# Performance work log

Hardware: AMD Instinct MI355X
Metric: run time of the kernel (lower is better)

Reference implementation:

```python
import jax, jax.numpy as jnp
import numpy as np

B, N, M, K, C = 2, 4096, 4096, 32, 64
RADIUS = 0.08


def _ball_query(d2, radius, k):
    # d2: (B, N, M) squared distances. Returns (B, N, k) int32 indices of the
    # first k in-radius neighbors (in index order); empty slots are filled with
    # the first found neighbor (or 0 if none), matching standard ball_query.
    m = d2.shape[-1]
    mask = d2 < radius * radius
    ar = jnp.arange(m, dtype=jnp.int32)
    key = jnp.where(mask, ar, ar + m)          # in-radius indices sort first
    neg_vals, _ = jax.lax.top_k(-key, k)       # k smallest keys
    vals = -neg_vals
    valid = vals < m
    raw = vals % m
    fill = raw[..., :1]                        # first neighbor (0 if none)
    return jnp.where(valid, raw, fill)


def setup_inputs() -> dict:
    key = jax.random.key(0)
    ks = jax.random.split(key, 9)
    points = jax.random.uniform(ks[0], (B, 3, N), dtype=jnp.float32)
    knnpoints = jax.random.uniform(ks[1], (B, 3, M), dtype=jnp.float32)
    feat = jax.random.normal(ks[2], (B, C, M), dtype=jnp.float32)
    w1 = jax.random.normal(ks[3], (128, C + 4), dtype=jnp.float32) * 0.05
    b1 = jnp.zeros((128,), jnp.float32)
    w2 = jax.random.normal(ks[4], (64, 128), dtype=jnp.float32) * 0.05
    b2 = jnp.zeros((64,), jnp.float32)
    w3 = jax.random.normal(ks[5], (64, 64), dtype=jnp.float32) * 0.05
    b3 = jnp.zeros((64,), jnp.float32)
    return {"points": points, "knnpoints": knnpoints, "feat": feat,
            "w1": w1, "b1": b1, "w2": w2, "b2": b2, "w3": w3, "b3": b3}


def reference(points, knnpoints, feat, w1, b1, w2, b2, w3, b3):
    # pairwise squared distances (B, N, M), computed once and reused by
    # ball_query and ChamferLoss
    pe = jnp.sum(points ** 2, axis=1)                       # (B, N)
    ke = jnp.sum(knnpoints ** 2, axis=1)                    # (B, M)
    cross = jnp.einsum('bdn,bdm->bnm', points, knnpoints)
    d2 = jnp.maximum(pe[:, :, None] + ke[:, None, :] - 2.0 * cross, 0.0)

    idx = _ball_query(jax.lax.stop_gradient(d2), RADIUS, K)  # (B, N, K)

    # gather neighbor coords / features: knnpoints[j, :, idx[j]]
    nb = jax.vmap(lambda p, i: p[:, i])(knnpoints, idx)      # (B, 3, N, K)
    nf = jax.vmap(lambda f, i: f[:, i])(feat, idx)           # (B, C, N, K)

    # relation features (neighbor_feature): diff + squared distance
    diff = nb - points[:, :, :, None]                        # (B, 3, N, K)
    dist = jnp.sum(diff ** 2, axis=1, keepdims=True)         # (B, 1, N, K)
    x = jnp.concatenate([nf, diff, dist], axis=1)            # (B, C+4, N, K)

    # SharedMLP: 1x1 conv stacks + ReLU
    h = jax.nn.relu(jnp.einsum('oc,bcnk->bonk', w1, x) + b1[None, :, None, None])
    h = jax.nn.relu(jnp.einsum('oc,bcnk->bonk', w2, h) + b2[None, :, None, None])
    h = jax.nn.relu(jnp.einsum('oc,bcnk->bonk', w3, h) + b3[None, :, None, None])
    agg = jnp.sum(h, axis=3)                                 # (B, 64, N)

    # ChamferLoss between points and knnpoints
    cd = jnp.sqrt(1e-6 + d2)
    loss = jnp.min(cd, axis=1).mean() + jnp.min(cd, axis=2).mean()
    return agg, loss
```

## Files before the change

kernel.cpp:

```cpp
#include <hip/hip_runtime.h>
#include <cstdint>

#define BB 2
#define NN 4096
#define MM 4096
#define KK 32
#define CC 64
#define R2C 0.0064f

typedef _Float16 v8h __attribute__((ext_vector_type(8)));
typedef _Float16 v4h __attribute__((ext_vector_type(4)));
typedef float    v4f __attribute__((ext_vector_type(4)));

#define TC  64
#define XS  104
#define H1S 136
#define H2S 72

#define NBLK_COLMIN 512
#define NBLK_MLP    4096
#define NBLK_TOTAL  4608

__launch_bounds__(256)
__global__ void prep_kernel(const float* __restrict__ knn,
                            const float* __restrict__ feat,
                            const float* __restrict__ w1,
                            const float* __restrict__ w2,
                            const float* __restrict__ w3,
                            _Float16* __restrict__ featH,
                            _Float16* __restrict__ w1h,
                            _Float16* __restrict__ w2h,
                            _Float16* __restrict__ w3h,
                            float4* __restrict__ knnP) {
    __shared__ __align__(16) float tl[64][65];
    int t = threadIdx.x, blk = blockIdx.x;

    if (blk < 128) {
        int b = blk >> 6;
        int m0 = (blk & 63) * 64;
        int mi = t & 63, cq = t >> 6;
        const float* src = feat + (size_t)b * CC * MM;
#pragma unroll
        for (int r = 0; r < 16; ++r) {
            int c = cq * 16 + r;
            tl[mi][c] = src[(size_t)c * MM + m0 + mi];
        }
        __syncthreads();
        int ci = t & 63, mq = t >> 6;
        _Float16* dst = featH + ((size_t)b * MM + m0) * CC;
#pragma unroll
        for (int r = 0; r < 16; ++r) {
            int mm2 = mq * 16 + r;
            dst[(size_t)mm2 * CC + ci] = (_Float16)tl[mm2][ci];
        }
    } else if (blk < 176) {
        int tt = (blk - 128) * 256 + t;
        if (tt < 128 * 96) {
            int r = tt / 96, k = tt - r * 96;
            w1h[tt] = (_Float16)((k < 68) ? w1[r * 68 + k] : 0.0f);
        }
        if (tt < 64 * 128) w2h[tt] = (_Float16)w2[tt];
        if (tt < 64 * 64)  w3h[tt] = (_Float16)w3[tt];
    } else {
        int i0 = (blk - 176) * 256 + t;
#pragma unroll
        for (int j = 0; j < 4; ++j) {
            int i = i0 + 2048 * j;
            int b = i >> 12, m = i & (MM - 1);
            const float* kp = knn + (size_t)b * 3 * MM;
            float x = kp[m], y = kp[MM + m], z = kp[2 * MM + m];
            float e = __fadd_rn(__fadd_rn(__fmul_rn(x, x), __fmul_rn(y, y)),
                                __fmul_rn(z, z));
            knnP[i] = make_float4(x, y, z, e);
        }
    }
}

__launch_bounds__(256, 4)
__global__ void fused_kernel(const float* __restrict__ points,
                             const float4* __restrict__ knnP,
                             const _Float16* __restrict__ featH,
                             const _Float16* __restrict__ w1h, const float* __restrict__ b1,
                             const _Float16* __restrict__ w2h, const float* __restrict__ b2,
                             const _Float16* __restrict__ w3h, const float* __restrict__ b3,
                             float* __restrict__ lossbuf,
                             float* __restrict__ out) {
    __shared__ __align__(16) _Float16 SM[TC * XS + TC * H1S];
    _Float16* X  = SM;
    _Float16* H2 = SM;
    _Float16* H1 = SM + TC * XS;
    __shared__ int   lists[2][4][KK];
    __shared__ int   cnts[2][4];
    __shared__ int   sidx2[2][KK];
    __shared__ float wmin[2][4];

    int t = threadIdx.x;
    int w = t >> 6, lane = t & 63;
    int blk = blockIdx.x;

    if (blk < NBLK_COLMIN) {
        float4* tile = (float4*)SM;
        int m0 = blk * 16;
        int b = blk >> 8;
        const float* pp = points + (size_t)b * 3 * NN;
        const float4* kq = knnP + (size_t)b * MM;
        float4 Kp[4];
#pragma unroll
        for (int p = 0; p < 4; ++p)
            Kp[p] = kq[(m0 & (MM - 1)) + 4 * w + p];
        float mn[4] = {1e30f, 1e30f, 1e30f, 1e30f};

        for (int ch = 0; ch < 4; ++ch) {
            const float* px = pp + ch * 1024;
#pragma unroll
            for (int j = 0; j < 4; ++j) {
                int i = t + 256 * j;
                float x = px[i], y = px[NN + i], z = px[2 * NN + i];
                float e = __fadd_rn(__fadd_rn(__fmul_rn(x, x), __fmul_rn(y, y)),
                                    __fmul_rn(z, z));
                tile[i] = make_float4(x, y, z, e);
            }
            __syncthreads();
#pragma unroll 2
            for (int i = 0; i < 16; ++i) {
                float4 p4 = tile[i * 64 + lane];
#pragma unroll
                for (int p = 0; p < 4; ++p) {
                    float cross = __builtin_fmaf(p4.z, Kp[p].z,
                                  __builtin_fmaf(p4.y, Kp[p].y,
                                                 __fmul_rn(p4.x, Kp[p].x)));
                    float d2 = __fsub_rn(__fadd_rn(p4.w, Kp[p].w),
                                         __fmul_rn(2.0f, cross));
                    mn[p] = fminf(mn[p], d2);
                }
            }
            __syncthreads();
        }

        float lsum = 0.0f;
#pragma unroll
        for (int p = 0; p < 4; ++p) {
            float mv = mn[p];
            for (int off = 32; off > 0; off >>= 1)
                mv = fminf(mv, __shfl_xor(mv, off));
            lsum += sqrtf(1e-6f + fmaxf(mv, 0.0f));
        }
        if (lane == 0) wmin[0][w] = lsum;
        __syncthreads();
        if (t == 0)
            lossbuf[blk] = (wmin[0][0] + wmin[0][1] + wmin[0][2] + wmin[0][3])
                           * (1.0f / (BB * MM));
    } else {
        int point0 = (blk - NBLK_COLMIN) * 2;
        int b = point0 >> 12;
        int n0 = point0 & (NN - 1);
        const float* pp = points + (size_t)b * 3 * NN;
        const float4* kq = knnP + (size_t)b * MM;

        float4 P[2];
#pragma unroll
        for (int p = 0; p < 2; ++p) {
            int n = n0 + p;
            float x = pp[n], y = pp[NN + n], z = pp[2 * NN + n];
            float e = __fadd_rn(__fadd_rn(__fmul_rn(x, x), __fmul_rn(y, y)),
                                __fmul_rn(z, z));
            P[p] = make_float4(x, y, z, e);
        }
        int cnt[2] = {0, 0};
        float mn[2] = {1e30f, 1e30f};
        int mbase = w * 1024 + lane;
#pragma unroll 4
        for (int it = 0; it < 16; ++it) {
            int m = mbase + it * 64;
            float4 k4 = kq[m];
#pragma unroll
            for (int p = 0; p < 2; ++p) {
                float cross = __builtin_fmaf(P[p].z, k4.z,
                              __builtin_fmaf(P[p].y, k4.y,
                                             __fmul_rn(P[p].x, k4.x)));
                float d2 = __fsub_rn(__fadd_rn(P[p].w, k4.w),
                                     __fmul_rn(2.0f, cross));
                mn[p] = fminf(mn[p], d2);
                bool hit = d2 < R2C;
                unsigned long long mask = __ballot(hit);
                if (hit) {
                    int pos = cnt[p] + __builtin_amdgcn_mbcnt_hi(
                                 (unsigned)(mask >> 32),
                                 __builtin_amdgcn_mbcnt_lo((unsigned)mask, 0));
                    if (pos < KK) lists[p][w][pos] = m;
                }
                cnt[p] += __popcll(mask);
            }
        }
#pragma unroll
        for (int p = 0; p < 2; ++p) {
            if (lane == 0) cnts[p][w] = cnt[p];
            float mv = mn[p];
            for (int off = 32; off > 0; off >>= 1)
                mv = fminf(mv, __shfl_xor(mv, off));
            if (lane == 0) wmin[p][w] = mv;
        }
        __syncthreads();

        if (w == 0) {
            int p = lane >> 5, k = lane & 31;
            int c0 = cnts[p][0], c1 = cnts[p][1], c2 = cnts[p][2], c3 = cnts[p][3];
            int o1 = c0, o2 = o1 + c1, o3 = o2 + c2, total = o3 + c3;
            int fillv = 0;
            if (c0 > 0)      fillv = lists[p][0][0];
            else if (c1 > 0) fillv = lists[p][1][0];
            else if (c2 > 0) fillv = lists[p][2][0];
            else if (c3 > 0) fillv = lists[p][3][0];
            int src, base;
            if (k < o1)      { src = 0; base = 0;  }
            else if (k < o2) { src = 1; base = o1; }
            else if (k < o3) { src = 2; base = o2; }
            else             { src = 3; base = o3; }
            int v = (k < total) ? lists[p][src][k - base] : fillv;
            sidx2[p][k] = v;
            if (lane == 0) {
                float r0 = fminf(fminf(wmin[0][0], wmin[0][1]),
                                 fminf(wmin[0][2], wmin[0][3]));
                float r1 = fminf(fminf(wmin[1][0], wmin[1][1]),
                                 fminf(wmin[1][2], wmin[1][3]));
                lossbuf[blk] = (sqrtf(1e-6f + fmaxf(r0, 0.0f)) +
                                sqrtf(1e-6f + fmaxf(r1, 0.0f)))
                               * (1.0f / (BB * NN));
            }
        }
        __syncthreads();

        {
            int col = t >> 2, h = t & 3;
            int pl = col >> 5, kk = col & 31;
            int n = n0 + pl;
            int id = sidx2[pl][kk];
            const v8h* src = (const v8h*)(featH + ((size_t)(b * MM + id)) * CC) + h * 2;
            v8h f0 = src[0], f1 = src[1];
            v8h* dst = (v8h*)(X + col * XS) + h * 2;
            dst[0] = f0; dst[1] = f1;
            v8h mv = {(_Float16)0.f, (_Float16)0.f, (_Float16)0.f, (_Float16)0.f,
                      (_Float16)0.f, (_Float16)0.f, (_Float16)0.f, (_Float16)0.f};
            if (h == 0) {
                float4 Pm = pl ? P[1] : P[0];
                float4 k4 = kq[id];
                float dx = k4.x - Pm.x, dy = k4.y - Pm.y, dz = k4.z - Pm.z;
                float dd = __fadd_rn(__fadd_rn(__fmul_rn(dx, dx), __fmul_rn(dy, dy)),
                                     __fmul_rn(dz, dz));
                mv[0] = (_Float16)dx; mv[1] = (_Float16)dy;
                mv[2] = (_Float16)dz; mv[3] = (_Float16)dd;
            }
            *((v8h*)(X + col * XS + 64) + h) = mv;
        }

        int quad = lane >> 4, lc = lane & 15;

        v8h a1[2][3], a2[4], a3[2];
#pragma unroll
        for (int rt = 0; rt < 2; ++rt)
#pragma unroll
            for (int ks = 0; ks < 3; ++ks)
                a1[rt][ks] = *(const v8h*)(w1h + (32 * w + 16 * rt + lc) * 96 + 32 * ks + 8 * quad);
#pragma unroll
        for (int ks = 0; ks < 4; ++ks)
            a2[ks] = *(const v8h*)(w2h + (16 * w + lc) * 128 + 32 * ks + 8 * quad);
#pragma unroll
        for (int ks = 0; ks < 2; ++ks)
            a3[ks] = *(const v8h*)(w3h + (16 * w + lc) * 64 + 32 * ks + 8 * quad);

        v4f bias1a = *(const v4f*)(b1 + 32 * w + 4 * quad);
        v4f bias1b = *(const v4f*)(b1 + 32 * w + 16 + 4 * quad);
        v4f bias2  = *(const v4f*)(b2 + 16 * w + 4 * quad);
        v4f bias3  = *(const v4f*)(b3 + 16 * w + 4 * quad);

        __syncthreads();

#pragma unroll 1
        for (int ct = 0; ct < 4; ++ct) {
            int colb = 16 * ct + lc;
            v4f acc0 = bias1a, acc1 = bias1b;
#pragma unroll
            for (int ks = 0; ks < 3; ++ks) {
                v8h bx = *(const v8h*)(X + colb * XS + 32 * ks + 8 * quad);
                acc0 = __builtin_amdgcn_mfma_f32_16x16x32_f16(a1[0][ks], bx, acc0, 0, 0, 0);
                acc1 = __builtin_amdgcn_mfma_f32_16x16x32_f16(a1[1][ks], bx, acc1, 0, 0, 0);
            }
            v4h h0, h1v;
#pragma unroll
            for (int r = 0; r < 4; ++r) {
                h0[r]  = (_Float16)fmaxf(acc0[r], 0.0f);
                h1v[r] = (_Float16)fmaxf(acc1[r], 0.0f);
            }
            *(v4h*)(H1 + colb * H1S + 32 * w + 4 * quad)      = h0;
            *(v4h*)(H1 + colb * H1S + 32 * w + 16 + 4 * quad) = h1v;
        }
        __syncthreads();

#pragma unroll 1
        for (int ct = 0; ct < 4; ++ct) {
            int colb = 16 * ct + lc;
            v4f acc = bias2;
#pragma unroll
            for (int ks = 0; ks < 4; ++ks) {
                v8h bx = *(const v8h*)(H1 + colb * H1S + 32 * ks + 8 * quad);
                acc = __builtin_amdgcn_mfma_f32_16x16x32_f16(a2[ks], bx, acc, 0, 0, 0);
            }
            v4h h;
#pragma unroll
            for (int r = 0; r < 4; ++r) h[r] = (_Float16)fmaxf(acc[r], 0.0f);
            *(v4h*)(H2 + colb * H2S + 16 * w + 4 * quad) = h;
        }
        __syncthreads();

#pragma unroll 1
        for (int p = 0; p < 2; ++p) {
            int cA = (2 * p) * 16 + lc, cB = (2 * p + 1) * 16 + lc;
            v4f accA = bias3, accB = bias3;
#pragma unroll
            for (int ks = 0; ks < 2; ++ks) {
                v8h bA = *(const v8h*)(H2 + cA * H2S + 32 * ks + 8 * quad);
                v8h bB = *(const v8h*)(H2 + cB * H2S + 32 * ks + 8 * quad);
                accA = __builtin_amdgcn_mfma_f32_16x16x32_f16(a3[ks], bA, accA, 0, 0, 0);
                accB = __builtin_amdgcn_mfma_f32_16x16x32_f16(a3[ks], bB, accB, 0, 0, 0);
            }
            v4f s;
#pragma unroll
            for (int r = 0; r < 4; ++r)
                s[r] = fmaxf(accA[r], 0.0f) + fmaxf(accB[r], 0.0f);
#pragma unroll
            for (int off = 1; off < 16; off <<= 1) {
#pragma unroll
                for (int r = 0; r < 4; ++r) s[r] += __shfl_xor(s[r], off);
            }
            if (lc == 0) {
                int n = n0 + p;
                int rowb = 16 * w + 4 * quad;
#pragma unroll
                for (int r = 0; r < 4; ++r)
                    out[((size_t)(b * 64 + rowb + r)) * NN + n] = s[r];
            }
        }
    }
}

__launch_bounds__(256)
__global__ void loss_kernel(const float* __restrict__ lossbuf,
                            float* __restrict__ out) {
    __shared__ float ws4[4];
    int t = threadIdx.x;
    float s = 0.0f;
#pragma unroll
    for (int q = 0; q < 18; ++q)
        s += lossbuf[t + 256 * q];
    for (int off = 32; off > 0; off >>= 1) s += __shfl_xor(s, off);
    if ((t & 63) == 0) ws4[t >> 6] = s;
    __syncthreads();
    if (t == 0)
        out[(size_t)BB * 64 * NN] = ws4[0] + ws4[1] + ws4[2] + ws4[3];
}

extern "C" void kernel_launch(void* const* d_in, const int* in_sizes, int n_in,
                              void* d_out, int out_size, void* d_ws, size_t ws_size,
                              hipStream_t stream) {
    const float* points = (const float*)d_in[0];
    const float* knn    = (const float*)d_in[1];
    const float* feat   = (const float*)d_in[2];
    const float* w1 = (const float*)d_in[3];
    const float* b1 = (const float*)d_in[4];
    const float* w2 = (const float*)d_in[5];
    const float* b2 = (const float*)d_in[6];
    const float* w3 = (const float*)d_in[7];
    const float* b3 = (const float*)d_in[8];
    float* out = (float*)d_out;

    char* ws = (char*)d_ws;
    _Float16*  featH   = (_Float16*)ws;
    _Float16*  w1h     = (_Float16*)(ws + 1048576);
    _Float16*  w2h     = (_Float16*)(ws + 1073152);
    _Float16*  w3h     = (_Float16*)(ws + 1089536);
    float4*    knnP    = (float4*)(ws + 1097728);
    float*     lossbuf = (float*)(ws + 1228800);

    prep_kernel<<<184, 256, 0, stream>>>(knn, feat, w1, w2, w3,
                                         featH, w1h, w2h, w3h, knnP);
    fused_kernel<<<NBLK_TOTAL, 256, 0, stream>>>(points, knnP, featH,
                                                 w1h, b1, w2h, b2, w3h, b3,
                                                 lossbuf, out);
    loss_kernel<<<1, 256, 0, stream>>>(lossbuf, out);
}
```

Measured before the change: 131.7 us.

## Load gathered features directly into MFMA operands, dropping the X staging tile

The fused kernel stops staging gathered neighbor features into a shared X tile. Each layer-1 MFMA now reads its B operand straight from global featH rows, and the relative-position metadata is precomputed by wave 0 into a small shared array. This removes the X buffer and one barrier, so shared memory shrinks and launch bounds rise to 5 blocks per CU. It also hoists the weight loads ahead of the ball query, merges the two ballots under a single branch, and vectorizes the featH transpose stores in prep. In exchange, each wave issues uncoalesced global loads inside the MFMA loop, and register pressure rises because the hoisted weights stay live through the search.

Result: no change. 132.6 us (+0.7%).

```diff
diff --git a/kernel.cpp b/kernel.cpp
--- a/kernel.cpp
+++ b/kernel.cpp
@@ -13,7 +13,6 @@
 typedef float    v4f __attribute__((ext_vector_type(4)));
 
 #define TC  64
-#define XS  104
 #define H1S 136
 #define H2S 72
 
@@ -46,12 +45,15 @@
             tl[mi][c] = src[(size_t)c * MM + m0 + mi];
         }
         __syncthreads();
-        int ci = t & 63, mq = t >> 6;
         _Float16* dst = featH + ((size_t)b * MM + m0) * CC;
 #pragma unroll
-        for (int r = 0; r < 16; ++r) {
-            int mm2 = mq * 16 + r;
-            dst[(size_t)mm2 * CC + ci] = (_Float16)tl[mm2][ci];
+        for (int rr = 0; rr < 2; ++rr) {
+            int mm2 = (t >> 3) + 32 * rr;
+            int cj = (t & 7) * 8;
+            v8h v;
+#pragma unroll
+            for (int j = 0; j < 8; ++j) v[j] = (_Float16)tl[mm2][cj + j];
+            *(v8h*)(dst + (size_t)mm2 * CC + cj) = v;
         }
     } else if (blk < 176) {
         int tt = (blk - 128) * 256 + t;
@@ -76,7 +78,7 @@
     }
 }
 
-__launch_bounds__(256, 4)
+__launch_bounds__(256, 5)
 __global__ void fused_kernel(const float* __restrict__ points,
                              const float4* __restrict__ knnP,
                              const _Float16* __restrict__ featH,
@@ -85,14 +87,14 @@
                              const _Float16* __restrict__ w3h, const float* __restrict__ b3,
                              float* __restrict__ lossbuf,
                              float* __restrict__ out) {
-    __shared__ __align__(16) _Float16 SM[TC * XS + TC * H1S];
-    _Float16* X  = SM;
-    _Float16* H2 = SM;
-    _Float16* H1 = SM + TC * XS;
+    __shared__ __align__(16) _Float16 SM[TC * H1S + TC * H2S];
+    _Float16* H1 = SM;
+    _Float16* H2 = SM + TC * H1S;
     __shared__ int   lists[2][4][KK];
     __shared__ int   cnts[2][4];
     __shared__ int   sidx2[2][KK];
     __shared__ float wmin[2][4];
+    __shared__ v4h   meta4[64];
 
     int t = threadIdx.x;
     int w = t >> 6, lane = t & 63;
@@ -157,6 +159,26 @@
         const float* pp = points + (size_t)b * 3 * NN;
         const float4* kq = knnP + (size_t)b * MM;
 
+        int quad = lane >> 4, lc = lane & 15;
+
+        v8h a1[2][3], a2[4], a3[2];
+#pragma unroll
+        for (int rt = 0; rt < 2; ++rt)
+#pragma unroll
+            for (int ks = 0; ks < 3; ++ks)
+                a1[rt][ks] = *(const v8h*)(w1h + (32 * w + 16 * rt + lc) * 96 + 32 * ks + 8 * quad);
+#pragma unroll
+        for (int ks = 0; ks < 4; ++ks)
+            a2[ks] = *(const v8h*)(w2h + (16 * w + lc) * 128 + 32 * ks + 8 * quad);
+#pragma unroll
+        for (int ks = 0; ks < 2; ++ks)
+            a3[ks] = *(const v8h*)(w3h + (16 * w + lc) * 64 + 32 * ks + 8 * quad);
+
+        v4f bias1a = *(const v4f*)(b1 + 32 * w + 4 * quad);
+        v4f bias1b = *(const v4f*)(b1 + 32 * w + 16 + 4 * quad);
+        v4f bias2  = *(const v4f*)(b2 + 16 * w + 4 * quad);
+        v4f bias3  = *(const v4f*)(b3 + 16 * w + 4 * quad);
+
         float4 P[2];
 #pragma unroll
         for (int p = 0; p < 2; ++p) {
@@ -173,23 +195,39 @@
         for (int it = 0; it < 16; ++it) {
             int m = mbase + it * 64;
             float4 k4 = kq[m];
-#pragma unroll
-            for (int p = 0; p < 2; ++p) {
-                float cross = __builtin_fmaf(P[p].z, k4.z,
-                              __builtin_fmaf(P[p].y, k4.y,
-                                             __fmul_rn(P[p].x, k4.x)));
-                float d2 = __fsub_rn(__fadd_rn(P[p].w, k4.w),
-                                     __fmul_rn(2.0f, cross));
-                mn[p] = fminf(mn[p], d2);
-                bool hit = d2 < R2C;
-                unsigned long long mask = __ballot(hit);
-                if (hit) {
-                    int pos = cnt[p] + __builtin_amdgcn_mbcnt_hi(
-                                 (unsigned)(mask >> 32),
-                                 __builtin_amdgcn_mbcnt_lo((unsigned)mask, 0));
-                    if (pos < KK) lists[p][w][pos] = m;
+            float d2a, d2b;
+            {
+                float cross = __builtin_fmaf(P[0].z, k4.z,
+                              __builtin_fmaf(P[0].y, k4.y,
+                                             __fmul_rn(P[0].x, k4.x)));
+                d2a = __fsub_rn(__fadd_rn(P[0].w, k4.w), __fmul_rn(2.0f, cross));
+            }
+            {
+                float cross = __builtin_fmaf(P[1].z, k4.z,
+                              __builtin_fmaf(P[1].y, k4.y,
+                                             __fmul_rn(P[1].x, k4.x)));
+                d2b = __fsub_rn(__fadd_rn(P[1].w, k4.w), __fmul_rn(2.0f, cross));
+            }
+            mn[0] = fminf(mn[0], d2a);
+            mn[1] = fminf(mn[1], d2b);
+            bool hit0 = d2a < R2C, hit1 = d2b < R2C;
+            unsigned long long mk0 = __ballot(hit0);
+            unsigned long long mk1 = __ballot(hit1);
+            if (mk0 | mk1) {
+                if (hit0) {
+                    int pos = cnt[0] + __builtin_amdgcn_mbcnt_hi(
+                                 (unsigned)(mk0 >> 32),
+                                 __builtin_amdgcn_mbcnt_lo((unsigned)mk0, 0));
+                    if (pos < KK) lists[0][w][pos] = m;
                 }
-                cnt[p] += __popcll(mask);
+                cnt[0] += __popcll(mk0);
+                if (hit1) {
+                    int pos = cnt[1] + __builtin_amdgcn_mbcnt_hi(
+                                 (unsigned)(mk1 >> 32),
+                                 __builtin_amdgcn_mbcnt_lo((unsigned)mk1, 0));
+                    if (pos < KK) lists[1][w][pos] = m;
+                }
+                cnt[1] += __popcll(mk1);
             }
         }
 #pragma unroll
@@ -218,6 +256,15 @@
             else             { src = 3; base = o3; }
             int v = (k < total) ? lists[p][src][k - base] : fillv;
             sidx2[p][k] = v;
+            float4 k4 = kq[v];
+            float4 Pm = p ? P[1] : P[0];
+            float dx = k4.x - Pm.x, dy = k4.y - Pm.y, dz = k4.z - Pm.z;
+            float dd = __fadd_rn(__fadd_rn(__fmul_rn(dx, dx), __fmul_rn(dy, dy)),
+                                 __fmul_rn(dz, dz));
+            v4h mv;
+            mv[0] = (_Float16)dx; mv[1] = (_Float16)dy;
+            mv[2] = (_Float16)dz; mv[3] = (_Float16)dd;
+            meta4[lane] = mv;
             if (lane == 0) {
                 float r0 = fminf(fminf(wmin[0][0], wmin[0][1]),
                                  fminf(wmin[0][2], wmin[0][3]));
@@ -230,61 +277,27 @@
         }
         __syncthreads();
 
-        {
-            int col = t >> 2, h = t & 3;
-            int pl = col >> 5, kk = col & 31;
-            int n = n0 + pl;
-            int id = sidx2[pl][kk];
-            const v8h* src = (const v8h*)(featH + ((size_t)(b * MM + id)) * CC) + h * 2;
-            v8h f0 = src[0], f1 = src[1];
-            v8h* dst = (v8h*)(X + col * XS) + h * 2;
-            dst[0] = f0; dst[1] = f1;
-            v8h mv = {(_Float16)0.f, (_Float16)0.f, (_Float16)0.f, (_Float16)0.f,
-                      (_Float16)0.f, (_Float16)0.f, (_Float16)0.f, (_Float16)0.f};
-            if (h == 0) {
-                float4 Pm = pl ? P[1] : P[0];
-                float4 k4 = kq[id];
-                float dx = k4.x - Pm.x, dy = k4.y - Pm.y, dz = k4.z - Pm.z;
-                float dd = __fadd_rn(__fadd_rn(__fmul_rn(dx, dx), __fmul_rn(dy, dy)),
-                                     __fmul_rn(dz, dz));
-                mv[0] = (_Float16)dx; mv[1] = (_Float16)dy;
-                mv[2] = (_Float16)dz; mv[3] = (_Float16)dd;
-            }
-            *((v8h*)(X + col * XS + 64) + h) = mv;
-        }
-
-        int quad = lane >> 4, lc = lane & 15;
-
-        v8h a1[2][3], a2[4], a3[2];
-#pragma unroll
-        for (int rt = 0; rt < 2; ++rt)
-#pragma unroll
-            for (int ks = 0; ks < 3; ++ks)
-                a1[rt][ks] = *(const v8h*)(w1h + (32 * w + 16 * rt + lc) * 96 + 32 * ks + 8 * quad);
-#pragma unroll
-        for (int ks = 0; ks < 4; ++ks)
-            a2[ks] = *(const v8h*)(w2h + (16 * w + lc) * 128 + 32 * ks + 8 * quad);
-#pragma unroll
-        for (int ks = 0; ks < 2; ++ks)
-            a3[ks] = *(const v8h*)(w3h + (16 * w + lc) * 64 + 32 * ks + 8 * quad);
-
-        v4f bias1a = *(const v4f*)(b1 + 32 * w + 4 * quad);
-        v4f bias1b = *(const v4f*)(b1 + 32 * w + 16 + 4 * quad);
-        v4f bias2  = *(const v4f*)(b2 + 16 * w + 4 * quad);
-        v4f bias3  = *(const v4f*)(b3 + 16 * w + 4 * quad);
-
-        __syncthreads();
-
 #pragma unroll 1
         for (int ct = 0; ct < 4; ++ct) {
             int colb = 16 * ct + lc;
+            int id = ((const int*)sidx2)[colb];
+            const _Float16* frow = featH + ((size_t)(b * MM + id)) * CC;
+            v8h bx0 = *(const v8h*)(frow + 8 * quad);
+            v8h bx1 = *(const v8h*)(frow + 32 + 8 * quad);
+            v4h mrow = meta4[colb];
+            v8h bx2 = {(_Float16)0.f, (_Float16)0.f, (_Float16)0.f, (_Float16)0.f,
+                       (_Float16)0.f, (_Float16)0.f, (_Float16)0.f, (_Float16)0.f};
+            if (quad == 0) {
+                bx2[0] = mrow[0]; bx2[1] = mrow[1];
+                bx2[2] = mrow[2]; bx2[3] = mrow[3];
+            }
             v4f acc0 = bias1a, acc1 = bias1b;
-#pragma unroll
-            for (int ks = 0; ks < 3; ++ks) {
-                v8h bx = *(const v8h*)(X + colb * XS + 32 * ks + 8 * quad);
-                acc0 = __builtin_amdgcn_mfma_f32_16x16x32_f16(a1[0][ks], bx, acc0, 0, 0, 0);
-                acc1 = __builtin_amdgcn_mfma_f32_16x16x32_f16(a1[1][ks], bx, acc1, 0, 0, 0);
-            }
+            acc0 = __builtin_amdgcn_mfma_f32_16x16x32_f16(a1[0][0], bx0, acc0, 0, 0, 0);
+            acc1 = __builtin_amdgcn_mfma_f32_16x16x32_f16(a1[1][0], bx0, acc1, 0, 0, 0);
+            acc0 = __builtin_amdgcn_mfma_f32_16x16x32_f16(a1[0][1], bx1, acc0, 0, 0, 0);
+            acc1 = __builtin_amdgcn_mfma_f32_16x16x32_f16(a1[1][1], bx1, acc1, 0, 0, 0);
+            acc0 = __builtin_amdgcn_mfma_f32_16x16x32_f16(a1[0][2], bx2, acc0, 0, 0, 0);
+            acc1 = __builtin_amdgcn_mfma_f32_16x16x32_f16(a1[1][2], bx2, acc1, 0, 0, 0);
             v4h h0, h1v;
 #pragma unroll
             for (int r = 0; r < 4; ++r) {
```

## Process 16 points per block with LDS-staged knn tiles and direct MLP gathers

Applied to the files above, without the earlier changes.

The heavy blocks now handle 16 query points each (one per wave quarter) instead of 2. knn coordinates are staged through shared memory in chunks so each wave scans all M points from LDS for 4 query points, with a skip when no lane hits. The ball-query result is compacted in place, and layer-1 MFMA operands are gathered straight from global featH instead of through an X staging tile. The prep kernel's feature transpose is also split across more, smaller blocks with vectorized half stores. Fewer blocks and more serial work per block trade parallelism for amortized knn loads and weight-fragment setup.

New measurement: 122.5 us. 7.0% less time.

```diff
diff --git a/kernel.cpp b/kernel.cpp
--- a/kernel.cpp
+++ b/kernel.cpp
@@ -12,14 +12,12 @@
 typedef _Float16 v4h __attribute__((ext_vector_type(4)));
 typedef float    v4f __attribute__((ext_vector_type(4)));
 
-#define TC  64
-#define XS  104
 #define H1S 136
 #define H2S 72
 
 #define NBLK_COLMIN 512
-#define NBLK_MLP    4096
-#define NBLK_TOTAL  4608
+#define NBLK_HEAVY  512
+#define NBLK_TOTAL  1024
 
 __launch_bounds__(256)
 __global__ void prep_kernel(const float* __restrict__ knn,
@@ -32,29 +30,30 @@
                             _Float16* __restrict__ w2h,
                             _Float16* __restrict__ w3h,
                             float4* __restrict__ knnP) {
-    __shared__ __align__(16) float tl[64][65];
+    __shared__ float tl[64][17];
     int t = threadIdx.x, blk = blockIdx.x;
 
-    if (blk < 128) {
-        int b = blk >> 6;
-        int m0 = (blk & 63) * 64;
-        int mi = t & 63, cq = t >> 6;
+    if (blk < 512) {
+        int b = blk >> 8;
+        int tb = blk & 255;
+        int c0 = (tb >> 6) * 16;
+        int m0 = (tb & 63) * 64;
         const float* src = feat + (size_t)b * CC * MM;
-#pragma unroll
-        for (int r = 0; r < 16; ++r) {
-            int c = cq * 16 + r;
-            tl[mi][c] = src[(size_t)c * MM + m0 + mi];
+        int mi = t & 63, cg = t >> 6;
+#pragma unroll
+        for (int r = 0; r < 4; ++r) {
+            int cl = cg * 4 + r;
+            tl[mi][cl] = src[(size_t)(c0 + cl) * MM + m0 + mi];
         }
         __syncthreads();
-        int ci = t & 63, mq = t >> 6;
-        _Float16* dst = featH + ((size_t)b * MM + m0) * CC;
-#pragma unroll
-        for (int r = 0; r < 16; ++r) {
-            int mm2 = mq * 16 + r;
-            dst[(size_t)mm2 * CC + ci] = (_Float16)tl[mm2][ci];
-        }
-    } else if (blk < 176) {
-        int tt = (blk - 128) * 256 + t;
+        int mm2 = t >> 2, j4 = (t & 3) * 4;
+        _Float16* dst = featH + ((size_t)b * MM + m0 + mm2) * CC + c0 + j4;
+        v4h v;
+#pragma unroll
+        for (int j = 0; j < 4; ++j) v[j] = (_Float16)tl[mm2][j4 + j];
+        *(v4h*)dst = v;
+    } else if (blk < 560) {
+        int tt = (blk - 512) * 256 + t;
         if (tt < 128 * 96) {
             int r = tt / 96, k = tt - r * 96;
             w1h[tt] = (_Float16)((k < 68) ? w1[r * 68 + k] : 0.0f);
@@ -62,7 +61,7 @@
         if (tt < 64 * 128) w2h[tt] = (_Float16)w2[tt];
         if (tt < 64 * 64)  w3h[tt] = (_Float16)w3[tt];
     } else {
-        int i0 = (blk - 176) * 256 + t;
+        int i0 = (blk - 560) * 256 + t;
 #pragma unroll
         for (int j = 0; j < 4; ++j) {
             int i = i0 + 2048 * j;
@@ -85,14 +84,13 @@
                              const _Float16* __restrict__ w3h, const float* __restrict__ b3,
                              float* __restrict__ lossbuf,
                              float* __restrict__ out) {
-    __shared__ __align__(16) _Float16 SM[TC * XS + TC * H1S];
-    _Float16* X  = SM;
-    _Float16* H2 = SM;
-    _Float16* H1 = SM + TC * XS;
-    __shared__ int   lists[2][4][KK];
-    __shared__ int   cnts[2][4];
-    __shared__ int   sidx2[2][KK];
-    __shared__ float wmin[2][4];
+    __shared__ __align__(16) _Float16 SM[64 * H1S + 64 * H2S];
+    _Float16* H1 = SM;
+    _Float16* H2 = SM + 64 * H1S;
+    __shared__ int    sidx_f[16][KK];
+    __shared__ v4h    meta[16][KK];
+    __shared__ float4 Plds[16];
+    __shared__ float  ws4[4];
 
     int t = threadIdx.x;
     int w = t >> 6, lane = t & 63;
@@ -145,113 +143,17 @@
                 mv = fminf(mv, __shfl_xor(mv, off));
             lsum += sqrtf(1e-6f + fmaxf(mv, 0.0f));
         }
-        if (lane == 0) wmin[0][w] = lsum;
+        if (lane == 0) ws4[w] = lsum;
         __syncthreads();
         if (t == 0)
-            lossbuf[blk] = (wmin[0][0] + wmin[0][1] + wmin[0][2] + wmin[0][3])
+            lossbuf[blk] = (ws4[0] + ws4[1] + ws4[2] + ws4[3])
                            * (1.0f / (BB * MM));
     } else {
-        int point0 = (blk - NBLK_COLMIN) * 2;
-        int b = point0 >> 12;
-        int n0 = point0 & (NN - 1);
+        int pt0 = (blk - NBLK_COLMIN) * 16;
+        int b = pt0 >> 12;
+        int n0 = pt0 & (NN - 1);
         const float* pp = points + (size_t)b * 3 * NN;
         const float4* kq = knnP + (size_t)b * MM;
-
-        float4 P[2];
-#pragma unroll
-        for (int p = 0; p < 2; ++p) {
-            int n = n0 + p;
-            float x = pp[n], y = pp[NN + n], z = pp[2 * NN + n];
-            float e = __fadd_rn(__fadd_rn(__fmul_rn(x, x), __fmul_rn(y, y)),
-                                __fmul_rn(z, z));
-            P[p] = make_float4(x, y, z, e);
-        }
-        int cnt[2] = {0, 0};
-        float mn[2] = {1e30f, 1e30f};
-        int mbase = w * 1024 + lane;
-#pragma unroll 4
-        for (int it = 0; it < 16; ++it) {
-            int m = mbase + it * 64;
-            float4 k4 = kq[m];
-#pragma unroll
-            for (int p = 0; p < 2; ++p) {
-                float cross = __builtin_fmaf(P[p].z, k4.z,
-                              __builtin_fmaf(P[p].y, k4.y,
-                                             __fmul_rn(P[p].x, k4.x)));
-                float d2 = __fsub_rn(__fadd_rn(P[p].w, k4.w),
-                                     __fmul_rn(2.0f, cross));
-                mn[p] = fminf(mn[p], d2);
-                bool hit = d2 < R2C;
-                unsigned long long mask = __ballot(hit);
-                if (hit) {
-                    int pos = cnt[p] + __builtin_amdgcn_mbcnt_hi(
-                                 (unsigned)(mask >> 32),
-                                 __builtin_amdgcn_mbcnt_lo((unsigned)mask, 0));
-                    if (pos < KK) lists[p][w][pos] = m;
-                }
-                cnt[p] += __popcll(mask);
-            }
-        }
-#pragma unroll
-        for (int p = 0; p < 2; ++p) {
-            if (lane == 0) cnts[p][w] = cnt[p];
-            float mv = mn[p];
-            for (int off = 32; off > 0; off >>= 1)
-                mv = fminf(mv, __shfl_xor(mv, off));
-            if (lane == 0) wmin[p][w] = mv;
-        }
-        __syncthreads();
-
-        if (w == 0) {
-            int p = lane >> 5, k = lane & 31;
-            int c0 = cnts[p][0], c1 = cnts[p][1], c2 = cnts[p][2], c3 = cnts[p][3];
-            int o1 = c0, o2 = o1 + c1, o3 = o2 + c2, total = o3 + c3;
-            int fillv = 0;
-            if (c0 > 0)      fillv = lists[p][0][0];
-            else if (c1 > 0) fillv = lists[p][1][0];
-            else if (c2 > 0) fillv = lists[p][2][0];
-            else if (c3 > 0) fillv = lists[p][3][0];
-            int src, base;
-            if (k < o1)      { src = 0; base = 0;  }
-            else if (k < o2) { src = 1; base = o1; }
-            else if (k < o3) { src = 2; base = o2; }
-            else             { src = 3; base = o3; }
-            int v = (k < total) ? lists[p][src][k - base] : fillv;
-            sidx2[p][k] = v;
-            if (lane == 0) {
-                float r0 = fminf(fminf(wmin[0][0], wmin[0][1]),
-                                 fminf(wmin[0][2], wmin[0][3]));
-                float r1 = fminf(fminf(wmin[1][0], wmin[1][1]),
-                                 fminf(wmin[1][2], wmin[1][3]));
-                lossbuf[blk] = (sqrtf(1e-6f + fmaxf(r0, 0.0f)) +
-                                sqrtf(1e-6f + fmaxf(r1, 0.0f)))
-                               * (1.0f / (BB * NN));
-            }
-        }
-        __syncthreads();
-
-        {
-            int col = t >> 2, h = t & 3;
-            int pl = col >> 5, kk = col & 31;
-            int n = n0 + pl;
-            int id = sidx2[pl][kk];
-            const v8h* src = (const v8h*)(featH + ((size_t)(b * MM + id)) * CC) + h * 2;
-            v8h f0 = src[0], f1 = src[1];
-            v8h* dst = (v8h*)(X + col * XS) + h * 2;
-            dst[0] = f0; dst[1] = f1;
-            v8h mv = {(_Float16)0.f, (_Float16)0.f, (_Float16)0.f, (_Float16)0.f,
-                      (_Float16)0.f, (_Float16)0.f, (_Float16)0.f, (_Float16)0.f};
-            if (h == 0) {
-                float4 Pm = pl ? P[1] : P[0];
-                float4 k4 = kq[id];
-                float dx = k4.x - Pm.x, dy = k4.y - Pm.y, dz = k4.z - Pm.z;
-                float dd = __fadd_rn(__fadd_rn(__fmul_rn(dx, dx), __fmul_rn(dy, dy)),
-                                     __fmul_rn(dz, dz));
-                mv[0] = (_Float16)dx; mv[1] = (_Float16)dy;
-                mv[2] = (_Float16)dz; mv[3] = (_Float16)dd;
-            }
-            *((v8h*)(X + col * XS + 64) + h) = mv;
-        }
 
         int quad = lane >> 4, lc = lane & 15;
 
@@ -273,72 +175,175 @@
         v4f bias2  = *(const v4f*)(b2 + 16 * w + 4 * quad);
         v4f bias3  = *(const v4f*)(b3 + 16 * w + 4 * quad);
 
+        float4 P[4];
+#pragma unroll
+        for (int p = 0; p < 4; ++p) {
+            int nl = n0 + 4 * w + p;
+            float x = pp[nl], y = pp[NN + nl], z = pp[2 * NN + nl];
+            float e = __fadd_rn(__fadd_rn(__fmul_rn(x, x), __fmul_rn(y, y)),
+                                __fmul_rn(z, z));
+            P[p] = make_float4(x, y, z, e);
+        }
+        if (lane == 0) {
+#pragma unroll
+            for (int p = 0; p < 4; ++p) Plds[4 * w + p] = P[p];
+        }
+
+        float4* tile = (float4*)SM;
+        int cnt[4] = {0, 0, 0, 0};
+        float mn[4] = {1e30f, 1e30f, 1e30f, 1e30f};
+
+        for (int ch = 0; ch < 4; ++ch) {
+#pragma unroll
+            for (int j = 0; j < 4; ++j) {
+                int i = t + 256 * j;
+                tile[i] = kq[ch * 1024 + i];
+            }
+            __syncthreads();
+#pragma unroll 2
+            for (int i = 0; i < 16; ++i) {
+                float4 k4 = tile[i * 64 + lane];
+                int m = ch * 1024 + i * 64 + lane;
+#pragma unroll
+                for (int p = 0; p < 4; ++p) {
+                    float cross = __builtin_fmaf(P[p].z, k4.z,
+                                  __builtin_fmaf(P[p].y, k4.y,
+                                                 __fmul_rn(P[p].x, k4.x)));
+                    float d2 = __fsub_rn(__fadd_rn(P[p].w, k4.w),
+                                         __fmul_rn(2.0f, cross));
+                    mn[p] = fminf(mn[p], d2);
+                    bool hit = d2 < R2C;
+                    unsigned long long mask = __ballot(hit);
+                    if (mask) {
+                        if (hit) {
+                            int pos = cnt[p] + __builtin_amdgcn_mbcnt_hi(
+                                         (unsigned)(mask >> 32),
+                                         __builtin_amdgcn_mbcnt_lo((unsigned)mask, 0));
+                            if (pos < KK) sidx_f[4 * w + p][pos] = m;
+                        }
+                        cnt[p] += __popcll(mask);
+                    }
+                }
+            }
+            __syncthreads();
+        }
+
+        float lsum = 0.0f;
+#pragma unroll
+        for (int p = 0; p < 4; ++p) {
+            int row = 4 * w + p;
+            if (lane < KK) {
+                int fillv = (cnt[p] > 0) ? sidx_f[row][0] : 0;
+                int v = (lane < cnt[p]) ? sidx_f[row][lane] : fillv;
+                sidx_f[row][lane] = v;
+            }
+            float mv = mn[p];
+            for (int off = 32; off > 0; off >>= 1)
+                mv = fminf(mv, __shfl_xor(mv, off));
+            lsum += sqrtf(1e-6f + fmaxf(mv, 0.0f));
+        }
+        if (lane == 0) ws4[w] = lsum;
         __syncthreads();
+        if (t == 0)
+            lossbuf[blk] = (ws4[0] + ws4[1] + ws4[2] + ws4[3])
+                           * (1.0f / (BB * NN));
+
+#pragma unroll
+        for (int c = t; c < 512; c += 256) {
+            int row = c >> 5, kk = c & 31;
+            int id = sidx_f[row][kk];
+            float4 k4 = kq[id];
+            float4 Pm = Plds[row];
+            float dx = k4.x - Pm.x, dy = k4.y - Pm.y, dz = k4.z - Pm.z;
+            float dd = __fadd_rn(__fadd_rn(__fmul_rn(dx, dx), __fmul_rn(dy, dy)),
+                                 __fmul_rn(dz, dz));
+            v4h mv;
+            mv[0] = (_Float16)dx; mv[1] = (_Float16)dy;
+            mv[2] = (_Float16)dz; mv[3] = (_Float16)dd;
+            meta[row][kk] = mv;
+        }
+        __syncthreads();
+
+        for (int q = 0; q < 8; ++q) {
+#pragma unroll 2
+            for (int ct = 0; ct < 4; ++ct) {
+                int colb = 16 * ct + lc;
+                int row = 2 * q + (ct >> 1);
+                int kk = colb & 31;
+                int id = sidx_f[row][kk];
+                const _Float16* frow = featH + ((size_t)(b * MM + id)) * CC;
+                v8h bx0 = *(const v8h*)(frow + 8 * quad);
+                v8h bx1 = *(const v8h*)(frow + 32 + 8 * quad);
+                v4h mr = meta[row][kk];
+                v8h bx2 = {(_Float16)0.f, (_Float16)0.f, (_Float16)0.f, (_Float16)0.f,
+                           (_Float16)0.f, (_Float16)0.f, (_Float16)0.f, (_Float16)0.f};
+                if (quad == 0) {
+                    bx2[0] = mr[0]; bx2[1] = mr[1];
+                    bx2[2] = mr[2]; bx2[3] = mr[3];
+                }
+                v4f acc0 = bias1a, acc1 = bias1b;
+                acc0 = __builtin_amdgcn_mfma_f32_16x16x32_f16(a1[0][0], bx0, acc0, 0, 0, 0);
+                acc1 = __builtin_amdgcn_mfma_f32_16x16x32_f16(a1[1][0], bx0, acc1, 0, 0, 0);
+                acc0 = __builtin_amdgcn_mfma_f32_16x16x32_f16(a1[0][1], bx1, acc0, 0, 0, 0);
+                acc1 = __builtin_amdgcn_mfma_f32_16x16x32_f16(a1[1][1], bx1, acc1, 0, 0, 0);
+                acc0 = __builtin_amdgcn_mfma_f32_16x16x32_f16(a1[0][2], bx2, acc0, 0, 0, 0);
+                acc1 = __builtin_amdgcn_mfma_f32_16x16x32_f16(a1[1][2], bx2, acc1, 0, 0, 0);
+                v4h h0, h1v;
+#pragma unroll
+                for (int r = 0; r < 4; ++r) {
+                    h0[r]  = (_Float16)fmaxf(acc0[r], 0.0f);
+                    h1v[r] = (_Float16)fmaxf(acc1[r], 0.0f);
+                }
+                *(v4h*)(H1 + colb * H1S + 32 * w + 4 * quad)      = h0;
+                *(v4h*)(H1 + colb * H1S + 32 * w + 16 + 4 * quad) = h1v;
+            }
+            __syncthreads();
 
 #pragma unroll 1
-        for (int ct = 0; ct < 4; ++ct) {
-            int colb = 16 * ct + lc;
-            v4f acc0 = bias1a, acc1 = bias1b;
-#pragma unroll
-            for (int ks = 0; ks < 3; ++ks) {
-                v8h bx = *(const v8h*)(X + colb * XS + 32 * ks + 8 * quad);
-                acc0 = __builtin_amdgcn_mfma_f32_16x16x32_f16(a1[0][ks], bx, acc0, 0, 0, 0);
-                acc1 = __builtin_amdgcn_mfma_f32_16x16x32_f16(a1[1][ks], bx, acc1, 0, 0, 0);
-            }
-            v4h h0, h1v;
-#pragma unroll
-            for (int r = 0; r < 4; ++r) {
-                h0[r]  = (_Float16)fmaxf(acc0[r], 0.0f);
-                h1v[r] = (_Float16)fmaxf(acc1[r], 0.0f);
-            }
-            *(v4h*)(H1 + colb * H1S + 32 * w + 4 * quad)      = h0;
-            *(v4h*)(H1 + colb * H1S + 32 * w + 16 + 4 * quad) = h1v;
-        }
-        __syncthreads();
+            for (int ct = 0; ct < 4; ++ct) {
+                int colb = 16 * ct + lc;
+                v4f acc = bias2;
+#pragma unroll
+                for (int ks = 0; ks < 4; ++ks) {
+                    v8h bx = *(const v8h*)(H1 + colb * H1S + 32 * ks + 8 * quad);
+                    acc = __builtin_amdgcn_mfma_f32_16x16x32_f16(a2[ks], bx, acc, 0, 0, 0);
+                }
+                v4h h;
+#pragma unroll
+                for (int r = 0; r < 4; ++r) h[r] = (_Float16)fmaxf(acc[r], 0.0f);
+                *(v4h*)(H2 + colb * H2S + 16 * w + 4 * quad) = h;
+            }
+            __syncthreads();
 
 #pragma unroll 1
-        for (int ct = 0; ct < 4; ++ct) {
-            int colb = 16 * ct + lc;
-            v4f acc = bias2;
-#pragma unroll
-            for (int ks = 0; ks < 4; ++ks) {
-                v8h bx = *(const v8h*)(H1 + colb * H1S + 32 * ks + 8 * quad);
-                acc = __builtin_amdgcn_mfma_f32_16x16x32_f16(a2[ks], bx, acc, 0, 0, 0);
-            }
-            v4h h;
-#pragma unroll
-            for (int r = 0; r < 4; ++r) h[r] = (_Float16)fmaxf(acc[r], 0.0f);
-            *(v4h*)(H2 + colb * H2S + 16 * w + 4 * quad) = h;
-        }
-        __syncthreads();
-
-#pragma unroll 1
-        for (int p = 0; p < 2; ++p) {
-            int cA = (2 * p) * 16 + lc, cB = (2 * p + 1) * 16 + lc;
-            v4f accA = bias3, accB = bias3;
-#pragma unroll
-            for (int ks = 0; ks < 2; ++ks) {
-                v8h bA = *(const v8h*)(H2 + cA * H2S + 32 * ks + 8 * quad);
-                v8h bB = *(const v8h*)(H2 + cB * H2S + 32 * ks + 8 * quad);
-                accA = __builtin_amdgcn_mfma_f32_16x16x32_f16(a3[ks], bA, accA, 0, 0, 0);
-                accB = __builtin_amdgcn_mfma_f32_16x16x32_f16(a3[ks], bB, accB, 0, 0, 0);
-            }
-            v4f s;
-#pragma unroll
-            for (int r = 0; r < 4; ++r)
-                s[r] = fmaxf(accA[r], 0.0f) + fmaxf(accB[r], 0.0f);
-#pragma unroll
-            for (int off = 1; off < 16; off <<= 1) {
-#pragma unroll
-                for (int r = 0; r < 4; ++r) s[r] += __shfl_xor(s[r], off);
-            }
-            if (lc == 0) {
-                int n = n0 + p;
-                int rowb = 16 * w + 4 * quad;
+            for (int p = 0; p < 2; ++p) {
+                int cA = (2 * p) * 16 + lc, cB = (2 * p + 1) * 16 + lc;
+                v4f accA = bias3, accB = bias3;
+#pragma unroll
+                for (int ks = 0; ks < 2; ++ks) {
+                    v8h bA = *(const v8h*)(H2 + cA * H2S + 32 * ks + 8 * quad);
+                    v8h bB = *(const v8h*)(H2 + cB * H2S + 32 * ks + 8 * quad);
+                    accA = __builtin_amdgcn_mfma_f32_16x16x32_f16(a3[ks], bA, accA, 0, 0, 0);
+                    accB = __builtin_amdgcn_mfma_f32_16x16x32_f16(a3[ks], bB, accB, 0, 0, 0);
+                }
+                v4f s;
 #pragma unroll
                 for (int r = 0; r < 4; ++r)
-                    out[((size_t)(b * 64 + rowb + r)) * NN + n] = s[r];
-            }
+                    s[r] = fmaxf(accA[r], 0.0f) + fmaxf(accB[r], 0.0f);
+#pragma unroll
+                for (int off = 1; off < 16; off <<= 1) {
+#pragma unroll
+                    for (int r = 0; r < 4; ++r) s[r] += __shfl_xor(s[r], off);
+                }
+                if (lc == 0) {
+                    int n = n0 + 2 * q + p;
+                    int rowb = 16 * w + 4 * quad;
+#pragma unroll
+                    for (int r = 0; r < 4; ++r)
+                        out[((size_t)(b * 64 + rowb + r)) * NN + n] = s[r];
+                }
+            }
+            __syncthreads();
         }
     }
 }
@@ -350,7 +355,7 @@
     int t = threadIdx.x;
     float s = 0.0f;
 #pragma unroll
-    for (int q = 0; q < 18; ++q)
+    for (int q = 0; q < 4; ++q)
         s += lossbuf[t + 256 * q];
     for (int off = 32; off > 0; off >>= 1) s += __shfl_xor(s, off);
     if ((t & 63) == 0) ws4[t >> 6] = s;
@@ -381,7 +386,7 @@
     float4*    knnP    = (float4*)(ws + 1097728);
     float*     lossbuf = (float*)(ws + 1228800);
 
-    prep_kernel<<<184, 256, 0, stream>>>(knn, feat, w1, w2, w3,
+    prep_kernel<<<568, 256, 0, stream>>>(knn, feat, w1, w2, w3,
                                          featH, w1h, w2h, w3h, knnP);
     fused_kernel<<<NBLK_TOTAL, 256, 0, stream>>>(points, knnP, featH,
                                                  w1h, b1, w2h, b2, w3h, b3,
```
